# Performance work log

Measured on AMD Instinct MI355X. Metric: run time of the kernel, lower is better.

## Reference

```python
import jax, jax.numpy as jnp
import numpy as np

N = 197          # tokens (== token_count)
B = 64           # batch
D = 768          # d_model
NH = 12          # n_head
GH = 2           # global_heads
HR = NH // GH    # head_ratio = 6
DH = 64          # d_head
QK = GH * DH     # qk_dim = 128
ML = 3           # mask_levels
EPS = 1e-5


def setup_inputs() -> dict:
    key = jax.random.key(0)
    ks = jax.random.split(key, 9)
    s = 1.0 / np.sqrt(D)
    return {
        "h": jax.random.normal(ks[0], (N, B, D), dtype=jnp.float32),
        "masks": jax.random.uniform(ks[1], (N, N, ML), dtype=jnp.float32),
        "Wq": jax.random.normal(ks[2], (QK, D), dtype=jnp.float32) * s,
        "Wk": jax.random.normal(ks[3], (QK, D), dtype=jnp.float32) * s,
        "Wv": jax.random.normal(ks[4], (NH * DH, D), dtype=jnp.float32) * s,
        "Wo": jax.random.normal(ks[5], (D, NH * DH), dtype=jnp.float32) * s,
        "mask_proj": jnp.ones((ML, NH), dtype=jnp.float32),
        "ln_gamma": jnp.ones((D,), dtype=jnp.float32),
        "ln_beta": jnp.zeros((D,), dtype=jnp.float32),
    }


def reference(h, masks, Wq, Wk, Wv, Wo, mask_proj, ln_gamma, ln_beta):
    scale = 1.0 / np.sqrt(DH)
    # projections (seq-first layout [N, B, ...])
    q = (h @ Wq.T).reshape(N, B, GH, DH)
    k = (h @ Wk.T).reshape(N, B, GH, DH)
    v = (h @ Wv.T).reshape(N, B, NH, DH)
    # global-head scores: [B, GH, i, j]
    score = jnp.einsum('ibgd,jbgd->bgij', q, k) * scale
    # learned mask mix: [i, j, NH] -> [GH, i, j, HR] (g-major head split, matches torch reshape)
    mw = jnp.einsum('ijl,ln->ijn', masks, mask_proj)
    mw = mw.reshape(N, N, GH, HR).transpose(2, 0, 1, 3)
    # broadcast each global head to HR local heads: [B, GH, i, j, HR]
    attn = score[..., None] * mw[None]
    attn = attn.transpose(0, 1, 4, 2, 3).reshape(B, NH, N, N)  # head = g*HR + r
    prob = jax.nn.softmax(attn, axis=-1)
    # AV: [i, B, NH, DH] -> [N, B, NH*DH]
    vec = jnp.einsum('bnij,jbnd->ibnd', prob, v).reshape(N, B, NH * DH)
    out = vec @ Wo.T
    # post-LN residual
    x = h + out
    mu = jnp.mean(x, axis=-1, keepdims=True)
    var = jnp.var(x, axis=-1, keepdims=True)
    return ln_gamma * (x - mu) / jnp.sqrt(var + EPS) + ln_beta
```

## Files before the change

kernel.cpp:

```cpp
#include <hip/hip_runtime.h>
#include <hip/hip_bf16.h>
#include <stdint.h>

#define NTOK 197
#define NPAD 224
#define BATCH 64
#define DMODEL 768
#define NHEAD 12
#define GHEAD 2
#define HRATIO 6
#define DHEAD 64
#define QKDIM 128
#define LNEPS 1e-5f
#define MROWS (NTOK * BATCH)
#define MPAD 12672
#define NKC 24
#define NBAND 99

using f32x4 = __attribute__((ext_vector_type(4))) float;
using s16x8 = __attribute__((ext_vector_type(8))) short;
using s16x4 = __attribute__((ext_vector_type(4))) short;

__device__ __forceinline__ short f2bf(float f) {
  unsigned int x = __float_as_uint(f);
  return (short)((x + 0x7fffu + ((x >> 16) & 1u)) >> 16);
}

__device__ __forceinline__ float bf2f(short s) {
  return __uint_as_float((unsigned)(unsigned short)s << 16);
}

__device__ __forceinline__ void gld16(void* lds, const void* g) {
  __builtin_amdgcn_global_load_lds(
      (const __attribute__((address_space(1))) unsigned int*)g,
      (__attribute__((address_space(3))) unsigned int*)lds, 16, 0, 0);
}

#define NBH (NBAND * NKC)
#define NBQ (8 * NKC)
#define NBW (6 * NKC)
__global__ __launch_bounds__(256)
void prep_kernel(const float* __restrict__ h, const float* __restrict__ Wq,
                 const float* __restrict__ Wk, const float* __restrict__ Wv,
                 const float* __restrict__ Wo, short* __restrict__ hf,
                 short* __restrict__ Wqkvf, short* __restrict__ Wof) {
  const int bb = blockIdx.x, t = threadIdx.x;
  int band, kc, which;
  if (bb < NBH) { which = 0; band = bb / NKC; kc = bb - band * NKC; }
  else if (bb < NBH + NBQ) { int i = bb - NBH; which = 1; band = i / NKC; kc = i - band * NKC; }
  else { int i = bb - NBH - NBQ; which = 2; band = i / NKC; kc = i - band * NKC; }
  short* dstS = (which == 0 ? hf : which == 1 ? Wqkvf : Wof) +
                ((size_t)(band * NKC + kc) * 8) * 512;
#pragma unroll
  for (int uu = 0; uu < 2; ++uu) {
    int u = t + uu * 256;
    int frag = u >> 6, l = u & 63;
    int rl = frag * 16 + (l & 15);
    int k0 = kc * 32 + ((l >> 4) & 3) * 8;
    float4 a = {0, 0, 0, 0}, c = {0, 0, 0, 0};
    if (which == 0) {
      int row = band * 128 + rl;
      if (row < MROWS) {
        const float* p = h + (size_t)row * DMODEL + k0;
        a = *(const float4*)p; c = *(const float4*)(p + 4);
      }
    } else if (which == 1) {
      int row = band * 128 + rl;
      const float* src = (row < 128) ? Wq + (size_t)row * DMODEL
                       : (row < 256) ? Wk + (size_t)(row - 128) * DMODEL
                                     : Wv + (size_t)(row - 256) * DMODEL;
      a = *(const float4*)(src + k0); c = *(const float4*)(src + k0 + 4);
    } else {
      const float* p = Wo + (size_t)(band * 128 + rl) * DMODEL + k0;
      a = *(const float4*)p; c = *(const float4*)(p + 4);
    }
    s16x8 o;
    o[0] = f2bf(a.x); o[1] = f2bf(a.y); o[2] = f2bf(a.z); o[3] = f2bf(a.w);
    o[4] = f2bf(c.x); o[5] = f2bf(c.y); o[6] = f2bf(c.z); o[7] = f2bf(c.w);
    *(s16x8*)(dstS + (size_t)u * 8) = o;
  }
}

template<int AM>
__global__ __launch_bounds__(256, 3)
void gemm_bstage_kernel(const short* __restrict__ Af, const short* __restrict__ Bf,
                        short* __restrict__ Cout, int M, int NC) {
  __shared__ short Bs[12 * 4 * 512];
  const int tid = threadIdx.x;
  const int nwg = gridDim.x * gridDim.y;
  const int orig = blockIdx.y * gridDim.x + blockIdx.x;
  const int qq = nwg >> 3, rr = nwg & 7;
  const int xcd = orig & 7, sidx = orig >> 3;
  const int wg = (xcd < rr ? xcd * (qq + 1) : rr * (qq + 1) + (xcd - rr) * qq) + sidx;
  const int cb = wg % gridDim.x;
  const int rb = wg / gridDim.x;

  const int w = tid >> 6, l = tid & 63;
  const int lm = l & 15, lh = l >> 4;

  const short* Bg = Bf + (size_t)(cb >> 1) * NKC * 4096 +
                    ((cb & 1) * 4 + w) * 512 + l * 8;
  const short* paF = Af + (size_t)rb * NKC * 4096 + (2 * w) * 512 + l * 8;
  const short* paR = Af + (size_t)(rb * 128 + w * 32 + lm) * DMODEL + lh * 8;

  f32x4 acc[2][4] = {};

#pragma unroll
  for (int half = 0; half < 2; ++half) {
    if (half) __syncthreads();
#pragma unroll
    for (int p = 0; p < 12; ++p)
      gld16(Bs + (p * 4 + w) * 512 + l * 8, Bg + (size_t)(half * 12 + p) * 4096);
    __syncthreads();
#pragma unroll
    for (int kcl = 0; kcl < 12; ++kcl) {
      const int kc = half * 12 + kcl;
      s16x8 af[2], bf[4];
      if (AM == 0) {
#pragma unroll
        for (int m = 0; m < 2; ++m)
          af[m] = *(const s16x8*)(paF + (size_t)kc * 4096 + m * 512);
      } else {
#pragma unroll
        for (int m = 0; m < 2; ++m)
          af[m] = *(const s16x8*)(paR + (size_t)m * 16 * DMODEL + kc * 32);
      }
#pragma unroll
      for (int n = 0; n < 4; ++n)
        bf[n] = *(const s16x8*)(Bs + (kcl * 4 + n) * 512 + l * 8);
#pragma unroll
      for (int m = 0; m < 2; ++m)
#pragma unroll
        for (int n = 0; n < 4; ++n)
          acc[m][n] = __builtin_amdgcn_mfma_f32_16x16x32_bf16(af[m], bf[n],
                                                              acc[m][n], 0, 0, 0);
    }
  }

#pragma unroll
  for (int m = 0; m < 2; ++m) {
#pragma unroll
    for (int r = 0; r < 4; ++r) {
      int row = rb * 128 + w * 32 + m * 16 + lh * 4 + r;
      if (row < M) {
#pragma unroll
        for (int n = 0; n < 4; ++n) {
          int col = cb * 64 + n * 16 + lm;
          Cout[(size_t)row * NC + col] = f2bf(acc[m][n][r]);
        }
      }
    }
  }
}

__global__ __launch_bounds__(256)
void packall_kernel(const short* __restrict__ Cb, const float* __restrict__ masks,
                    const float* __restrict__ mproj, short* __restrict__ qp,
                    short* __restrict__ kp, short* __restrict__ vT,
                    short* __restrict__ mwb) {
  __shared__ short Vs[NPAD][DHEAD + 1];
  const int bb = blockIdx.x, t = threadIdx.x;
  if (bb < 256) {
    int b = bb >> 2, g = (bb >> 1) & 1, which = bb & 1;
    short* dst = (which ? kp : qp) + ((size_t)b * GHEAD + g) * NPAD * 64;
    int d = t & 63, iofs = t >> 6;
    for (int i0 = 0; i0 < NPAD; i0 += 4) {
      int i = i0 + iofs;
      short v = 0;
      if (i < NTOK)
        v = Cb[(size_t)(i * BATCH + b) * 1024 + which * QKDIM + g * DHEAD + d];
      int dd = which ? ((((d >> 3) ^ (i & 7)) << 3) | (d & 7)) : d;
      dst[i * 64 + dd] = v;
    }
  } else if (bb < 1024) {
    int vv = bb - 256;
    int b = vv / 12, n = vv - b * 12;
    int d = t & 63, iofs = t >> 6;
    for (int i0 = 0; i0 < NPAD; i0 += 4) {
      int i = i0 + iofs;
      short v = 0;
      if (i < NTOK)
        v = Cb[(size_t)(i * BATCH + b) * 1024 + 256 + n * DHEAD + d];
      Vs[i][d] = v;
    }
    __syncthreads();
    short* dst = vT + ((size_t)b * NHEAD + n) * DHEAD * NPAD;
    int sub = t & 63, dr = t >> 6;
    for (int d0 = 0; d0 < DHEAD; d0 += 4) {
      if (sub < 56) {
        int dd = d0 + dr, j0 = sub * 4;
        s16x4 o;
        o[0] = Vs[j0][dd]; o[1] = Vs[j0 + 1][dd];
        o[2] = Vs[j0 + 2][dd]; o[3] = Vs[j0 + 3][dd];
        *(s16x4*)(dst + dd * NPAD + j0) = o;
      }
    }
  } else {
    int e = (bb - 1024) * 256 + t;
    int n = e >> 12;
    int rem = e & 4095;
    int i = rem >> 4, lm = rem & 15;
    float p0 = mproj[n], p1 = mproj[NHEAD + n], p2 = mproj[2 * NHEAD + n];
    float vals[16];
#pragma unroll
    for (int jf = 0; jf < 16; ++jf) vals[jf] = 0.f;
    if (i < NTOK) {
#pragma unroll
      for (int jf = 0; jf < 14; ++jf) {
        int col = jf * 16 + lm;
        if (col < NTOK) {
          const float* mp = masks + ((size_t)i * NTOK + col) * 3;
          vals[jf] = 0.125f * (mp[0] * p0 + mp[1] * p1 + mp[2] * p2);
        }
      }
    }
    s16x8 o0, o1;
#pragma unroll
    for (int q = 0; q < 8; ++q) { o0[q] = f2bf(vals[q]); o1[q] = f2bf(vals[8 + q]); }
    short* dst = mwb + (size_t)e * 16;
    *(s16x8*)dst = o0;
    *(s16x8*)(dst + 8) = o1;
  }
}

__global__ __launch_bounds__(256, 2)
void attn_fused_kernel(const short* __restrict__ qp, const short* __restrict__ kp,
                       const short* __restrict__ vT, const short* __restrict__ mwb,
                       short* __restrict__ vec_b) {
  const int lin = blockIdx.x;
  const int it = lin & 3, g = (lin >> 2) & 1, b = lin >> 3;
  __shared__ short Ks[NPAD * 64];
  __shared__ short Pt[64 * 256];
  __shared__ float rsb[64];
  const int t = threadIdx.x, w = t >> 6, l = t & 63;
  const int lm = l & 15, lh = l >> 4, l7 = l & 7;

  const short* qg = qp + ((size_t)b * GHEAD + g) * NPAD * 64;
  const short* kg = kp + ((size_t)b * GHEAD + g) * NPAD * 64;

#pragma unroll
  for (int s = 0; s < 7; ++s)
    gld16(Ks + s * 2048 + t * 8, kg + s * 2048 + t * 8);
  int qrow = it * 64 + w * 16 + lm;
  if (qrow > NPAD - 1) qrow = NPAD - 1;
  s16x8 a0 = *(const s16x8*)(qg + qrow * 64 + lh * 8);
  s16x8 a1 = *(const s16x8*)(qg + qrow * 64 + 32 + lh * 8);
  __syncthreads();

  f32x4 acc[14] = {};
#pragma unroll
  for (int jf = 0; jf < 14; ++jf) {
    s16x8 kf0 = *(const s16x8*)((const char*)Ks + (jf * 16 + lm) * 128 + ((lh ^ l7) << 4));
    s16x8 kf1 = *(const s16x8*)((const char*)Ks + (jf * 16 + lm) * 128 + (((4 + lh) ^ l7) << 4));
    acc[jf] = __builtin_amdgcn_mfma_f32_16x16x32_bf16(a0, kf0, acc[jf], 0, 0, 0);
    acc[jf] = __builtin_amdgcn_mfma_f32_16x16x32_bf16(a1, kf1, acc[jf], 0, 0, 0);
  }

  for (int hh = 0; hh < HRATIO; ++hh) {
    const int n = g * HRATIO + hh;
    const short* vg = vT + ((size_t)b * NHEAD + n) * 64 * NPAD;
    s16x8 vf[7];
#pragma unroll
    for (int ks = 0; ks < 7; ++ks)
      vf[ks] = *(const s16x8*)(vg + (w * 16 + lm) * NPAD + ks * 32 + lh * 8);

#pragma unroll
    for (int r = 0; r < 4; ++r) {
      const int row = w * 16 + lh * 4 + r;
      const int i = it * 64 + row;
      const short* mr = mwb + (((size_t)n * 256 + i) * 16 + lm) * 16;
      s16x8 mh0 = *(const s16x8*)(mr);
      s16x8 mh1 = *(const s16x8*)(mr + 8);
      float sum = 0.f;
#pragma unroll
      for (int jf = 0; jf < 13; ++jf) {
        float mwv = bf2f((jf < 8) ? mh0[jf] : mh1[jf - 8]);
        float pe = __expf(acc[jf][r] * mwv);
        if (jf == 12 && lm >= 5) pe = 0.f;
        sum += pe;
        int byteoff = row * 512 + (((2 * jf + (lm >> 3)) ^ (row & 7)) << 4) + (lm & 7) * 2;
        *(short*)((char*)Pt + byteoff) = f2bf(pe);
      }
      {
        int byteoff = row * 512 + (((26 + (lm >> 3)) ^ (row & 7)) << 4) + (lm & 7) * 2;
        *(short*)((char*)Pt + byteoff) = 0;
      }
#pragma unroll
      for (int off = 8; off; off >>= 1) sum += __shfl_xor(sum, off);
      if (lm == 0) rsb[row] = 1.f / sum;
    }
    __syncthreads();

    __builtin_amdgcn_s_setprio(1);
    f32x4 oacc[4] = {};
#pragma unroll
    for (int fi = 0; fi < 4; ++fi)
#pragma unroll
      for (int ks = 0; ks < 7; ++ks) {
        s16x8 pa = *(const s16x8*)((const char*)Pt + (fi * 16 + lm) * 512 +
                                   (((ks * 4 + lh) ^ l7) << 4));
        oacc[fi] = __builtin_amdgcn_mfma_f32_16x16x32_bf16(pa, vf[ks], oacc[fi], 0, 0, 0);
      }
    __builtin_amdgcn_s_setprio(0);
#pragma unroll
    for (int fi = 0; fi < 4; ++fi)
#pragma unroll
      for (int r = 0; r < 4; ++r) {
        int ia = it * 64 + fi * 16 + lh * 4 + r;
        if (ia < NTOK) {
          float rsv = rsb[fi * 16 + lh * 4 + r];
          vec_b[((size_t)ia * BATCH + b) * DMODEL + n * 64 + w * 16 + lm] =
              f2bf(oacc[fi][r] * rsv);
        }
      }
    __syncthreads();
  }
}

__global__ __launch_bounds__(256)
void ln_kernel(const float* __restrict__ h, const short* __restrict__ proj_b,
               float* __restrict__ out, const float* __restrict__ gamma,
               const float* __restrict__ beta) {
  const int m = blockIdx.x;
  const float* hrow = h + (size_t)m * DMODEL;
  const short* prow = proj_b + (size_t)m * DMODEL;
  float* orow = out + (size_t)m * DMODEL;
  const int tid = threadIdx.x;
  float v0 = hrow[tid] + bf2f(prow[tid]);
  float v1 = hrow[tid + 256] + bf2f(prow[tid + 256]);
  float v2 = hrow[tid + 512] + bf2f(prow[tid + 512]);
  float s = v0 + v1 + v2;
  float sq = v0 * v0 + v1 * v1 + v2 * v2;
#pragma unroll
  for (int off = 32; off; off >>= 1) {
    s += __shfl_xor(s, off);
    sq += __shfl_xor(sq, off);
  }
  __shared__ float ss[4], ssq[4];
  const int w = tid >> 6, lane = tid & 63;
  if (lane == 0) { ss[w] = s; ssq[w] = sq; }
  __syncthreads();
  s = ss[0] + ss[1] + ss[2] + ss[3];
  sq = ssq[0] + ssq[1] + ssq[2] + ssq[3];
  const float inv = 1.0f / (float)DMODEL;
  float mu = s * inv;
  float var = sq * inv - mu * mu;
  float rstd = rsqrtf(var + LNEPS);
  orow[tid] = gamma[tid] * (v0 - mu) * rstd + beta[tid];
  orow[tid + 256] = gamma[tid + 256] * (v1 - mu) * rstd + beta[tid + 256];
  orow[tid + 512] = gamma[tid + 512] * (v2 - mu) * rstd + beta[tid + 512];
}

extern "C" void kernel_launch(void* const* d_in, const int* in_sizes, int n_in,
                              void* d_out, int out_size, void* d_ws, size_t ws_size,
                              hipStream_t stream) {
  const float* h     = (const float*)d_in[0];
  const float* masks = (const float*)d_in[1];
  const float* Wq    = (const float*)d_in[2];
  const float* Wk    = (const float*)d_in[3];
  const float* Wv    = (const float*)d_in[4];
  const float* Wo    = (const float*)d_in[5];
  const float* mproj = (const float*)d_in[6];
  const float* gamma = (const float*)d_in[7];
  const float* beta  = (const float*)d_in[8];
  float* out = (float*)d_out;

  char* ws = (char*)d_ws;
  size_t o = 0;
  auto alloc = [&](size_t bytes) { size_t r = o; o += (bytes + 255) & ~(size_t)255; return r; };
  short* hf    = (short*)(ws + alloc((size_t)MPAD * DMODEL * 2));
  short* Cb    = (short*)(ws + alloc((size_t)MPAD * 1024 * 2));
  short* Wqkvf = (short*)(ws + alloc((size_t)1024 * DMODEL * 2));
  short* Wof   = (short*)(ws + alloc((size_t)DMODEL * DMODEL * 2));
  short* qp    = (short*)(ws + alloc((size_t)BATCH * GHEAD * NPAD * DHEAD * 2));
  short* kp    = (short*)(ws + alloc((size_t)BATCH * GHEAD * NPAD * DHEAD * 2));
  short* vT    = (short*)(ws + alloc((size_t)BATCH * NHEAD * DHEAD * NPAD * 2));
  short* mwb   = (short*)(ws + alloc((size_t)NHEAD * 256 * 16 * 16 * 2));
  short* vec_b = hf;
  short* proj_b = Cb;

  prep_kernel<<<NBH + NBQ + NBW, 256, 0, stream>>>(h, Wq, Wk, Wv, Wo, hf, Wqkvf, Wof);
  gemm_bstage_kernel<0><<<dim3(1024 / 64, NBAND), 256, 0, stream>>>(
      hf, Wqkvf, Cb, MROWS, 1024);
  packall_kernel<<<1216, 256, 0, stream>>>(Cb, masks, mproj, qp, kp, vT, mwb);
  attn_fused_kernel<<<512, 256, 0, stream>>>(qp, kp, vT, mwb, vec_b);
  gemm_bstage_kernel<1><<<dim3(DMODEL / 64, NBAND), 256, 0, stream>>>(
      vec_b, Wof, proj_b, MROWS, DMODEL);
  ln_kernel<<<MROWS, 256, 0, stream>>>(h, proj_b, out, gamma, beta);
}
```

Baseline: 150.3 us.

## Double-buffer B tile staging in GEMM to overlap loads with MFMA

Replaces the two-phase stage-then-compute loop over halves of K with a four-step ping-pong pipeline over two LDS buffers. Each step prefetches the next quarter of B with async global-to-LDS loads while the current quarter feeds the MFMAs, using explicit vmcnt and lgkmcnt waits and raw barriers. The aim is to hide the global load latency that was previously exposed before each half. LDS size is unchanged. The hand-tuned waitcnt counts depend on how the compiler orders the A-fragment global loads, which risks stalls or races if that ordering changes.

```diff
diff --git a/kernel.cpp b/kernel.cpp
--- a/kernel.cpp
+++ b/kernel.cpp
@@ -85,7 +85,7 @@
 __global__ __launch_bounds__(256, 3)
 void gemm_bstage_kernel(const short* __restrict__ Af, const short* __restrict__ Bf,
                         short* __restrict__ Cout, int M, int NC) {
-  __shared__ short Bs[12 * 4 * 512];
+  __shared__ short Bs[2][6 * 4 * 512];
   const int tid = threadIdx.x;
   const int nwg = gridDim.x * gridDim.y;
   const int orig = blockIdx.y * gridDim.x + blockIdx.x;
@@ -105,29 +105,37 @@
 
   f32x4 acc[2][4] = {};
 
-#pragma unroll
-  for (int half = 0; half < 2; ++half) {
-    if (half) __syncthreads();
-#pragma unroll
-    for (int p = 0; p < 12; ++p)
-      gld16(Bs + (p * 4 + w) * 512 + l * 8, Bg + (size_t)(half * 12 + p) * 4096);
-    __syncthreads();
-#pragma unroll
-    for (int kcl = 0; kcl < 12; ++kcl) {
-      const int kc = half * 12 + kcl;
+#define STAGEQ(buf, qt)                                                       \
+  do {                                                                        \
+    _Pragma("unroll") for (int p = 0; p < 6; ++p)                             \
+      gld16(&Bs[buf][(p * 4 + w) * 512 + l * 8],                              \
+            Bg + (size_t)((qt) * 6 + p) * 4096);                              \
+  } while (0)
+
+  STAGEQ(0, 0);
+  for (int qt = 0; qt < 4; ++qt) {
+    const int cur = qt & 1;
+    if (qt + 1 < 4) {
+      STAGEQ(cur ^ 1, qt + 1);
+      asm volatile("s_waitcnt vmcnt(6)" ::: "memory");
+    } else {
+      asm volatile("s_waitcnt vmcnt(0)" ::: "memory");
+    }
+    __builtin_amdgcn_s_barrier();
+#pragma unroll
+    for (int kcl = 0; kcl < 6; ++kcl) {
+      const int kc = qt * 6 + kcl;
       s16x8 af[2], bf[4];
       if (AM == 0) {
-#pragma unroll
-        for (int m = 0; m < 2; ++m)
-          af[m] = *(const s16x8*)(paF + (size_t)kc * 4096 + m * 512);
+        af[0] = *(const s16x8*)(paF + (size_t)kc * 4096);
+        af[1] = *(const s16x8*)(paF + (size_t)kc * 4096 + 512);
       } else {
-#pragma unroll
-        for (int m = 0; m < 2; ++m)
-          af[m] = *(const s16x8*)(paR + (size_t)m * 16 * DMODEL + kc * 32);
+        af[0] = *(const s16x8*)(paR + (size_t)kc * 32);
+        af[1] = *(const s16x8*)(paR + 16 * DMODEL + (size_t)kc * 32);
       }
 #pragma unroll
       for (int n = 0; n < 4; ++n)
-        bf[n] = *(const s16x8*)(Bs + (kcl * 4 + n) * 512 + l * 8);
+        bf[n] = *(const s16x8*)(&Bs[cur][(kcl * 4 + n) * 512 + l * 8]);
 #pragma unroll
       for (int m = 0; m < 2; ++m)
 #pragma unroll
@@ -135,7 +143,10 @@
           acc[m][n] = __builtin_amdgcn_mfma_f32_16x16x32_bf16(af[m], bf[n],
                                                               acc[m][n], 0, 0, 0);
     }
-  }
+    asm volatile("s_waitcnt lgkmcnt(0)" ::: "memory");
+    __builtin_amdgcn_s_barrier();
+  }
+#undef STAGEQ
 
 #pragma unroll
   for (int m = 0; m < 2; ++m) {
```

New measurement: 151.5 us. No clear change (+0.8%).
